# Kernel optimization log

Measured on AMD Instinct MI355X. Metric: run time of the kernel, lower is better.

## Reference

```python
import jax, jax.numpy as jnp
import numpy as np

# Static configuration (uniform ragged layout: every sequence has the same lengths)
B = 8          # number of sequences
QLEN = 256     # new query tokens per sequence
D = 1024       # embedding_dim
H = 16         # num_attention_heads
HD = D // H    # head dim = 64
FFN = 4096     # ffn_embedding_dim
PAGE = 16      # KV-cache page size
KV_TOTAL = 4096            # total KV length per sequence (prefix + new)
P = KV_TOTAL // PAGE       # pages per sequence = 256
NEW_PAGES = QLEN // PAGE   # pages occupied by the new tokens = 16
NUM_PAGES = B * P          # 2048
PREFIX = KV_TOTAL - QLEN   # cached prefix length per sequence
SCALE = HD ** -0.5
LN_EPS = 1e-5


def layer_norm(x, g, b):
    mu = jnp.mean(x, axis=-1, keepdims=True)
    var = jnp.mean(jnp.square(x - mu), axis=-1, keepdims=True)
    return (x - mu) * jax.lax.rsqrt(var + LN_EPS) * g + b


def setup_inputs() -> dict:
    key = jax.random.key(0)
    ks = jax.random.split(key, 12)
    s = 0.02
    inp = {
        "x": jax.random.normal(ks[0], (B * QLEN, D), jnp.float32),
        "pagetable": jax.random.normal(ks[1], (NUM_PAGES, 2, PAGE, H, HD), jnp.float32) * 0.5,
        "Wq": jax.random.normal(ks[2], (D, D), jnp.float32) * s,
        "bq": jnp.zeros((D,), jnp.float32),
        "Wk": jax.random.normal(ks[3], (D, D), jnp.float32) * s,
        "bk": jnp.zeros((D,), jnp.float32),
        "Wv": jax.random.normal(ks[4], (D, D), jnp.float32) * s,
        "bv": jnp.zeros((D,), jnp.float32),
        "Wo": jax.random.normal(ks[5], (D, D), jnp.float32) * s,
        "bo": jnp.zeros((D,), jnp.float32),
        "ln1_g": jnp.ones((D,), jnp.float32),
        "ln1_b": jnp.zeros((D,), jnp.float32),
        "W1": jax.random.normal(ks[6], (D, FFN), jnp.float32) * s,
        "b1": jnp.zeros((FFN,), jnp.float32),
        "W2": jax.random.normal(ks[7], (FFN, D), jnp.float32) * s,
        "b2": jnp.zeros((D,), jnp.float32),
        "lnf_g": jnp.ones((D,), jnp.float32),
        "lnf_b": jnp.zeros((D,), jnp.float32),
        "qo_indptr": jnp.arange(B + 1, dtype=jnp.int32) * QLEN,
        "paged_kv_indptr": jnp.arange(B + 1, dtype=jnp.int32) * P,
        "paged_kv_indices": jnp.arange(NUM_PAGES, dtype=jnp.int32),
        "paged_kv_last_page_len": jnp.full((B,), PAGE, jnp.int32),
        "layer_idx": 0,
    }
    return inp


def reference(x, pagetable, Wq, bq, Wk, bk, Wv, bv, Wo, bo,
              ln1_g, ln1_b, W1, b1, W2, b2, lnf_g, lnf_b,
              qo_indptr, paged_kv_indptr, paged_kv_indices,
              paged_kv_last_page_len, layer_idx):
    residual = x

    # ---- paged self-attention (post-LN path: layer_norm_first=False) ----
    q = ((x @ Wq + bq) * SCALE).reshape(B, QLEN, H, HD)
    k_new = (x @ Wk + bk).reshape(B, QLEN, H, HD)
    v_new = (x @ Wv + bv).reshape(B, QLEN, H, HD)

    # append new K/V into the last NEW_PAGES pages of each sequence
    page_ids = paged_kv_indices.reshape(B, P)                 # [B, P]
    new_ids = page_ids[:, P - NEW_PAGES:].reshape(-1)         # [B*NEW_PAGES]
    kv_new = jnp.stack([k_new, v_new], axis=2)                # [B, QLEN, 2, H, HD]
    kv_new = kv_new.reshape(B, NEW_PAGES, PAGE, 2, H, HD).transpose(0, 1, 3, 2, 4, 5)
    pt = pagetable.at[new_ids].set(kv_new.reshape(-1, 2, PAGE, H, HD))

    # gather the full paged KV per sequence
    kv = pt[page_ids]                                         # [B, P, 2, PAGE, H, HD]
    K = kv[:, :, 0].reshape(B, KV_TOTAL, H, HD)
    V = kv[:, :, 1].reshape(B, KV_TOTAL, H, HD)

    # streaming-causal mask: query i attends to kv positions <= PREFIX + i
    scores = jnp.einsum("bqhd,bkhd->bhqk", q, K)              # [B, H, QLEN, KV_TOTAL]
    kv_pos = jnp.arange(KV_TOTAL)[None, :]
    q_pos = PREFIX + jnp.arange(QLEN)[:, None]
    scores = jnp.where(kv_pos <= q_pos, scores, jnp.float32(-1e30))
    attn = jax.nn.softmax(scores, axis=-1)
    ctx = jnp.einsum("bhqk,bkhd->bqhd", attn, V).reshape(B * QLEN, D)
    x = ctx @ Wo + bo

    x = residual + x
    x = layer_norm(x, ln1_g, ln1_b)

    # ---- FFN ----
    residual = x
    x = jax.nn.relu(x @ W1 + b1)
    x = x @ W2 + b2
    layer_result = x
    x = residual + x
    x = layer_norm(x, lnf_g, lnf_b)

    return x, layer_result, pt
```

## Files before the change

kernel.cpp:

```cpp
#include <hip/hip_runtime.h>
#include <hip/hip_bf16.h>

typedef unsigned short u16;
typedef __attribute__((ext_vector_type(4))) float f32x4;
typedef __attribute__((ext_vector_type(8))) short short8;

#define MODE_QKV 0
#define MODE_WO  1
#define MODE_F1  2
#define MODE_F2  3

__device__ inline u16 f2bf(float f) {
    __hip_bfloat16 h = __float2bfloat16(f);
    return *(u16*)&h;
}

typedef __attribute__((address_space(3))) unsigned int lds_u32_t;
typedef const __attribute__((address_space(1))) unsigned int glb_u32_t;
__device__ inline void gload16(const u16* g, u16* l) {
    __builtin_amdgcn_global_load_lds((glb_u32_t*)(const void*)g,
                                     (lds_u32_t*)(void*)l, 16, 0, 0);
}

__global__ __launch_bounds__(256) void prep_wx(
    const float* __restrict__ Wq, const float* __restrict__ Wk,
    const float* __restrict__ Wv, const float* __restrict__ x,
    u16* __restrict__ WqkvT, u16* __restrict__ xb) {
    int bid = blockIdx.x;
    int tid = threadIdx.x;
    int tx = tid & 31, ty = tid >> 5;
    if (bid >= 3072) {
        int i = (bid - 3072) * 256 + tid;
        const float4* p = (const float4*)(x + (size_t)i * 8);
        float4 a = p[0], b = p[1];
        u16 t[8] = {f2bf(a.x), f2bf(a.y), f2bf(a.z), f2bf(a.w),
                    f2bf(b.x), f2bf(b.y), f2bf(b.z), f2bf(b.w)};
        *(uint4*)(xb + (size_t)i * 8) = *(const uint4*)t;
        return;
    }
    int m = bid >> 10, r = bid & 1023;
    const float* src = (m == 0) ? Wq : (m == 1) ? Wk : Wv;
    u16* dst = WqkvT + (size_t)m * 1024 * 1024;
    __shared__ float t[32][33];
    int n0 = (r & 31) * 32, k0 = (r >> 5) * 32;
#pragma unroll
    for (int j = 0; j < 32; j += 8)
        t[ty + j][tx] = src[(size_t)(k0 + ty + j) * 1024 + n0 + tx];
    __syncthreads();
#pragma unroll
    for (int j = 0; j < 32; j += 8)
        dst[(size_t)(n0 + ty + j) * 1024 + k0 + tx] = f2bf(t[tx][ty + j]);
}

__global__ __launch_bounds__(256) void ln_wo(const float* __restrict__ p0,
                                             const float* __restrict__ p1,
                                             const float* __restrict__ bo,
                                             const float* __restrict__ resid,
                                             const float* __restrict__ g,
                                             const float* __restrict__ be,
                                             float* __restrict__ outf,
                                             u16* __restrict__ outb) {
    int row = blockIdx.x;
    int tid = threadIdx.x;
    int c = tid * 4;
    size_t o = (size_t)row * 1024 + c;
    f32x4 v = *(const f32x4*)(p0 + o) + *(const f32x4*)(p1 + o)
            + *(const f32x4*)(bo + c) + *(const f32x4*)(resid + o);
    float s = v[0] + v[1] + v[2] + v[3];
#pragma unroll
    for (int m = 1; m < 64; m <<= 1) s += __shfl_xor(s, m, 64);
    __shared__ float red1[4], red2[4];
    int w = tid >> 6;
    if ((tid & 63) == 0) red1[w] = s;
    __syncthreads();
    float mu = (red1[0] + red1[1] + red1[2] + red1[3]) * (1.0f / 1024.0f);
    f32x4 d = v - mu;
    float q = d[0] * d[0] + d[1] * d[1] + d[2] * d[2] + d[3] * d[3];
#pragma unroll
    for (int m = 1; m < 64; m <<= 1) q += __shfl_xor(q, m, 64);
    if ((tid & 63) == 0) red2[w] = q;
    __syncthreads();
    float var = (red2[0] + red2[1] + red2[2] + red2[3]) * (1.0f / 1024.0f);
    float rs = rsqrtf(var + 1e-5f);
    f32x4 gg = *(const f32x4*)(g + c), bb = *(const f32x4*)(be + c);
    f32x4 ov = d * rs * gg + bb;
    *(f32x4*)(outf + o) = ov;
    u16 t[4] = {f2bf(ov[0]), f2bf(ov[1]), f2bf(ov[2]), f2bf(ov[3])};
    *(uint2*)&outb[o] = *(const uint2*)t;
}

__global__ __launch_bounds__(256) void ln_f2(const float* __restrict__ q0,
                                             const float* __restrict__ b2,
                                             const float* __restrict__ xln1f,
                                             const float* __restrict__ g,
                                             const float* __restrict__ be,
                                             float* __restrict__ out_lr,
                                             float* __restrict__ out_x) {
    int row = blockIdx.x;
    int tid = threadIdx.x;
    int c = tid * 4;
    size_t o = (size_t)row * 1024 + c;
    const size_t st = (size_t)2048 * 1024;
    f32x4 v = *(const f32x4*)(q0 + o) + *(const f32x4*)(q0 + st + o)
            + *(const f32x4*)(q0 + 2 * st + o) + *(const f32x4*)(q0 + 3 * st + o)
            + *(const f32x4*)(b2 + c);
    *(f32x4*)(out_lr + o) = v;
    v = v + *(const f32x4*)(xln1f + o);
    float s = v[0] + v[1] + v[2] + v[3];
#pragma unroll
    for (int m = 1; m < 64; m <<= 1) s += __shfl_xor(s, m, 64);
    __shared__ float red1[4], red2[4];
    int w = tid >> 6;
    if ((tid & 63) == 0) red1[w] = s;
    __syncthreads();
    float mu = (red1[0] + red1[1] + red1[2] + red1[3]) * (1.0f / 1024.0f);
    f32x4 d = v - mu;
    float q = d[0] * d[0] + d[1] * d[1] + d[2] * d[2] + d[3] * d[3];
#pragma unroll
    for (int m = 1; m < 64; m <<= 1) q += __shfl_xor(q, m, 64);
    if ((tid & 63) == 0) red2[w] = q;
    __syncthreads();
    float var = (red2[0] + red2[1] + red2[2] + red2[3]) * (1.0f / 1024.0f);
    float rs = rsqrtf(var + 1e-5f);
    f32x4 gg = *(const f32x4*)(g + c), bb = *(const f32x4*)(be + c);
    *(f32x4*)(out_x + o) = d * rs * gg + bb;
}

template <int MODE>
__device__ __forceinline__ void gemm_body(
    u16* As, u16* Bs, int m0, int n0,
    const u16* __restrict__ A, const u16* __restrict__ Bt, int lda, int Kspan, int N,
    const float* __restrict__ bias0, const float* __restrict__ bias1,
    const float* __restrict__ bias2,
    float* __restrict__ o0, u16* __restrict__ ob,
    u16* __restrict__ kbf, u16* __restrict__ vbf, const int* __restrict__ kvidx) {
    int tid = threadIdx.x;
    int l = tid & 63, w = tid >> 6;
    int wr = w >> 1, wc = w & 1;
    int lr = l & 15, lg = l >> 4;
    int lrow8 = l >> 3;
    int scol = ((l & 7) ^ lrow8) << 3;
    f32x4 acc[4][4] = {};
    for (int kb = 0; kb < Kspan; kb += 64) {
#pragma unroll
        for (int p = 0; p < 4; ++p) {
            int chunk = p * 4 + w;
            int r = chunk * 8 + lrow8;
            gload16(&A[(size_t)(m0 + r) * lda + kb + scol], &As[chunk * 512]);
            gload16(&Bt[(size_t)(n0 + r) * lda + kb + scol], &Bs[chunk * 512]);
        }
        __syncthreads();
#pragma unroll
        for (int kk = 0; kk < 2; ++kk) {
            short8 a[4], b[4];
            int c0 = kk * 32 + lg * 8;
#pragma unroll
            for (int mi = 0; mi < 4; mi++) {
                int row = wr * 64 + mi * 16 + lr;
                a[mi] = *(const short8*)&As[row * 64 + (c0 ^ ((row & 7) << 3))];
            }
#pragma unroll
            for (int ni = 0; ni < 4; ni++) {
                int row = wc * 64 + ni * 16 + lr;
                b[ni] = *(const short8*)&Bs[row * 64 + (c0 ^ ((row & 7) << 3))];
            }
#pragma unroll
            for (int mi = 0; mi < 4; mi++)
#pragma unroll
                for (int ni = 0; ni < 4; ni++)
                    acc[mi][ni] = __builtin_amdgcn_mfma_f32_16x16x32_bf16(
                        a[mi], b[ni], acc[mi][ni], 0, 0, 0);
        }
        __syncthreads();
    }
#pragma unroll
    for (int mi = 0; mi < 4; mi++) {
#pragma unroll
        for (int ni = 0; ni < 4; ni++) {
#pragma unroll
            for (int r = 0; r < 4; r++) {
                int row = m0 + wr * 64 + mi * 16 + lg * 4 + r;
                int col = n0 + wc * 64 + ni * 16 + lr;
                float v = acc[mi][ni][r];
                if constexpr (MODE == MODE_QKV) {
                    int sel = col >> 10, c = col & 1023;
                    int b = row >> 8, ii = row & 255;
                    int h = (c >> 6), hd = c & 63;
                    if (sel == 0) {
                        ob[(size_t)row * 1024 + c] = f2bf((v + bias0[c]) * 0.125f);
                    } else if (sel == 1) {
                        float val = v + bias1[c];
                        int page = kvidx[b * 256 + 240 + (ii >> 4)];
                        o0[(size_t)page * 32768 + (size_t)(ii & 15) * 1024 + c] = val;
                        kbf[((size_t)(b * 16 + h) * 4096 + 3840 + ii) * 64 + hd] = f2bf(val);
                    } else {
                        float val = v + bias2[c];
                        int page = kvidx[b * 256 + 240 + (ii >> 4)];
                        o0[(size_t)page * 32768 + 16384 + (size_t)(ii & 15) * 1024 + c] = val;
                        vbf[((size_t)(b * 16 + h) * 64 + hd) * 4096 + 3840 + ii] = f2bf(val);
                    }
                } else if constexpr (MODE == MODE_F1) {
                    float t = v + bias0[col];
                    ob[(size_t)row * N + col] = f2bf(fmaxf(t, 0.0f));
                } else {
                    o0[(size_t)row * N + col] = v;
                }
            }
        }
    }
}

template <int MODE>
__global__ __launch_bounds__(256) void gemm_nt(
    const u16* __restrict__ A, const u16* __restrict__ Bt,
    int lda, int Kspan, int N, int gx, int nper,
    const float* __restrict__ bias0,
    float* __restrict__ o0, u16* __restrict__ ob, size_t osplit) {
    __shared__ __align__(16) u16 smem[128 * 64 * 2];
    int bid = blockIdx.x;
    int split = bid / nper, t = bid % nper;
    gemm_body<MODE>(smem, smem + 128 * 64, (t / gx) * 128, (t % gx) * 128,
                    A + (size_t)split * Kspan, Bt + (size_t)split * Kspan,
                    lda, Kspan, N, bias0, nullptr, nullptr,
                    o0 ? o0 + (size_t)split * osplit : nullptr, ob,
                    nullptr, nullptr, nullptr);
}

__global__ __launch_bounds__(256) void mega_prep(
    const u16* __restrict__ xb, const u16* __restrict__ WqkvT,
    const float* __restrict__ bq, const float* __restrict__ bk,
    const float* __restrict__ bv,
    float* __restrict__ out_pt, u16* __restrict__ qbuf,
    u16* __restrict__ Kbf, u16* __restrict__ Vtbf,
    const float* __restrict__ pgt, const int* __restrict__ kvidx,
    const float* __restrict__ Wo, const float* __restrict__ W1,
    const float* __restrict__ W2,
    u16* __restrict__ WoT, u16* __restrict__ W1T, u16* __restrict__ W2T) {
    __shared__ __align__(16) u16 smem[128 * 64 * 2];
    int bid = blockIdx.x;
    int tid = threadIdx.x;
    if (bid < 480) {
        int tile = bid % 60, b = bid / 60;
        int T0 = tile * 64;
        int h = tid >> 4, hd0 = (tid & 15) * 4;
        int pg[4];
#pragma unroll
        for (int pi = 0; pi < 4; ++pi) pg[pi] = kvidx[b * 256 + (T0 >> 4) + pi];
#pragma unroll 4
        for (int it2 = 0; it2 < 64; ++it2) {
            int pi = it2 >> 4, it = it2 & 15;
            const float* src = pgt + (size_t)pg[pi] * 32768;
            float* dst = out_pt + (size_t)pg[pi] * 32768;
            size_t o = (size_t)it * 1024 + tid * 4;
            float4 f = *(const float4*)(src + o);
            *(float4*)(dst + o) = f;
            u16 k4[4] = {f2bf(f.x), f2bf(f.y), f2bf(f.z), f2bf(f.w)};
            size_t kdst = ((size_t)(b * 16 + h) * 4096 + T0 + pi * 16 + it) * 64 + hd0;
            *(uint2*)&Kbf[kdst] = *(const uint2*)k4;
        }
        return;
    }
    if (bid < 960) {
        int vb2 = bid - 480;
        int tile = vb2 % 60, b = vb2 / 60;
        int T0 = tile * 64;
        int pg[4];
#pragma unroll
        for (int pi = 0; pi < 4; ++pi) pg[pi] = kvidx[b * 256 + (T0 >> 4) + pi];
        u16* vt = smem;
        for (int hb2 = 0; hb2 < 8; ++hb2) {
#pragma unroll 4
            for (int it = 0; it < 8; ++it) {
                int ti = it * 8 + (tid >> 5);
                int pi = ti >> 4, tokloc = ti & 15;
                int c4 = (tid & 31) * 4;
                size_t o = (size_t)pg[pi] * 32768 + 16384 + (size_t)tokloc * 1024
                           + hb2 * 128 + c4;
                float4 v = *(const float4*)(pgt + o);
                *(float4*)(out_pt + o) = v;
                u16 v4[4] = {f2bf(v.x), f2bf(v.y), f2bf(v.z), f2bf(v.w)};
                *(uint2*)&vt[ti * 134 + c4] = *(const uint2*)v4;
            }
            __syncthreads();
            int g = tid >> 4, j = tid & 15;
#pragma unroll
            for (int rp = 0; rp < 8; ++rp) {
                int ri = rp * 16 + g;
                int h = hb2 * 2 + (ri >> 6), hd = ri & 63;
                u16 o4[4];
#pragma unroll
                for (int s = 0; s < 4; ++s) o4[s] = vt[(j * 4 + s) * 134 + ri];
                *(uint2*)&Vtbf[((size_t)(b * 16 + h) * 64 + hd) * 4096 + T0 + j * 4] =
                    *(const uint2*)o4;
            }
            __syncthreads();
        }
        return;
    }
    if (bid < 1344) {
        int t = bid - 960;
        gemm_body<MODE_QKV>(smem, smem + 8192, (t / 24) * 128, (t % 24) * 128,
                            xb, WqkvT, 1024, 1024, 3072, bq, bk, bv,
                            out_pt, qbuf, Kbf, Vtbf, kvidx);
        return;
    }
    int wb = bid - 1344;
    const float* src; u16* dst; int K, N, bx, by;
    if (wb < 1024) {
        bx = wb & 31; by = wb >> 5; K = 1024; N = 1024; src = Wo; dst = WoT;
    } else if (wb < 5120) {
        int r = wb - 1024; bx = r & 127; by = r >> 7; K = 1024; N = 4096; src = W1; dst = W1T;
    } else {
        int r = wb - 5120; bx = r & 31; by = r >> 5; K = 4096; N = 1024; src = W2; dst = W2T;
    }
    float* t = (float*)smem;
    int tx = tid & 31, ty = tid >> 5;
    int n0 = bx * 32, k0 = by * 32;
#pragma unroll
    for (int j = 0; j < 32; j += 8)
        t[(ty + j) * 33 + tx] = src[(size_t)(k0 + ty + j) * N + n0 + tx];
    __syncthreads();
#pragma unroll
    for (int j = 0; j < 32; j += 8)
        dst[(size_t)(n0 + ty + j) * K + k0 + tx] = f2bf(t[tx * 33 + ty + j]);
}

__global__ __launch_bounds__(512) void attn_kernel(const u16* __restrict__ qb,
                                                   const u16* __restrict__ Kbf,
                                                   const u16* __restrict__ Vtbf,
                                                   float* __restrict__ pOct,
                                                   float* __restrict__ pL) {
    __shared__ u16 Ks[64 * 64];
    __shared__ u16 Vt[64 * 64];
    __shared__ u16 Ps[8][16 * 64];
    int bid = blockIdx.x;
    int tid = threadIdx.x;
    int l = tid & 63, w = tid >> 6;
    int lr = l & 15, lg = l >> 4;
    int x = bid & 7, qt = x >> 2, split = x & 3;
    int h = (bid >> 3) & 15, b = bid >> 7;

    int qrow = qt * 128 + w * 16 + lr;
    const u16* qptr = qb + (size_t)(b * 256 + qrow) * 1024 + h * 64 + lg * 8;
    short8 qf0 = *(const short8*)qptr;
    short8 qf1 = *(const short8*)(qptr + 32);

    const u16* kslab = Kbf + (size_t)(b * 16 + h) * 4096 * 64;
    const u16* vslab = Vtbf + (size_t)(b * 16 + h) * 64 * 4096;

    f32x4 octx[4] = {};
    f32x4 lacc = {};
    short8 ones;
#pragma unroll
    for (int jj = 0; jj < 8; jj++) ones[jj] = (short)0x3F80;

    int qbase = 3840 + qt * 128;
    int ntiles = (qbase + 128) >> 6;
    int tstart = split * 16;
    int tend = min(tstart + 16, ntiles);
    int kt0 = tstart * 64, kt1 = tend * 64;

    int srow = tid >> 3, scol8 = (tid & 7) * 8;
    int sdst = srow * 64 + (scol8 ^ ((srow & 7) << 3));
    const u16* kp = kslab + srow * 64 + scol8;
    const u16* vp = vslab + (size_t)srow * 4096 + scol8;

    uint4 kreg = *(const uint4*)(kp + (size_t)kt0 * 64);
    uint4 vreg = *(const uint4*)(vp + kt0);
    for (int kt = kt0; kt < kt1; kt += 64) {
        *(uint4*)&Ks[sdst] = kreg;
        *(uint4*)&Vt[sdst] = vreg;
        __syncthreads();
        bool hn = (kt + 64) < kt1;
        if (hn) {
            kreg = *(const uint4*)(kp + (size_t)(kt + 64) * 64);
            vreg = *(const uint4*)(vp + kt + 64);
        }
        float P[4][4];
        bool need_mask = (kt + 63 > qbase);
#pragma unroll
        for (int ni = 0; ni < 4; ni++) {
            f32x4 s = {};
            int krow = ni * 16 + lr;
            int swz = (krow & 7) << 3;
            short8 k0 = *(const short8*)&Ks[krow * 64 + ((lg * 8) ^ swz)];
            short8 k1 = *(const short8*)&Ks[krow * 64 + ((32 + lg * 8) ^ swz)];
            s = __builtin_amdgcn_mfma_f32_16x16x32_bf16(qf0, k0, s, 0, 0, 0);
            s = __builtin_amdgcn_mfma_f32_16x16x32_bf16(qf1, k1, s, 0, 0, 0);
            if (need_mask) {
                int col = kt + ni * 16 + lr;
#pragma unroll
                for (int r = 0; r < 4; r++) {
                    int q = qt * 128 + w * 16 + lg * 4 + r;
                    P[ni][r] = (col <= 3840 + q) ? __expf(s[r]) : 0.0f;
                }
            } else {
#pragma unroll
                for (int r = 0; r < 4; r++) P[ni][r] = __expf(s[r]);
            }
        }
#pragma unroll
        for (int ni = 0; ni < 4; ni++)
#pragma unroll
            for (int r = 0; r < 4; r++) {
                int prow = lg * 4 + r;
                Ps[w][prow * 64 + ((ni * 16 + lr) ^ ((prow & 7) << 3))] = f2bf(P[ni][r]);
            }
#pragma unroll
        for (int kk = 0; kk < 2; kk++) {
            int c0 = kk * 32 + lg * 8;
            short8 pf = *(const short8*)&Ps[w][lr * 64 + (c0 ^ ((lr & 7) << 3))];
            lacc = __builtin_amdgcn_mfma_f32_16x16x32_bf16(pf, ones, lacc, 0, 0, 0);
#pragma unroll
            for (int dt = 0; dt < 4; dt++) {
                int vrow = dt * 16 + lr;
                short8 vf = *(const short8*)&Vt[vrow * 64 + (c0 ^ ((vrow & 7) << 3))];
                octx[dt] = __builtin_amdgcn_mfma_f32_16x16x32_bf16(pf, vf, octx[dt], 0, 0, 0);
            }
        }
        __syncthreads();
    }
    size_t obase = (((size_t)(split * 8 + b) * 16 + h) * 256 + qt * 128) * 64;
#pragma unroll
    for (int dt = 0; dt < 4; dt++)
#pragma unroll
        for (int r = 0; r < 4; r++)
            pOct[obase + (size_t)(w * 16 + lg * 4 + r) * 64 + dt * 16 + lr] = octx[dt][r];
    if (lr == 0) {
        size_t lbase = ((size_t)(split * 8 + b) * 16 + h) * 256 + qt * 128;
#pragma unroll
        for (int r = 0; r < 4; r++) pL[lbase + w * 16 + lg * 4 + r] = lacc[r];
    }
}

__global__ __launch_bounds__(256) void attn_combine(const float* __restrict__ pOct,
                                                    const float* __restrict__ pL,
                                                    u16* __restrict__ ctxb) {
    int row = blockIdx.x;
    int b = row >> 8, q = row & 255;
    int tid = threadIdx.x;
    int h = tid >> 4, dq = (tid & 15) * 4;
    size_t stride = (size_t)128 * 256 * 64;
    size_t base = ((size_t)(b * 16 + h) * 256 + q) * 64 + dq;
    size_t lstride = 128 * 256;
    size_t lbase = (size_t)(b * 16 + h) * 256 + q;
    f32x4 s = {};
    float ls = 0.0f;
#pragma unroll
    for (int sp = 0; sp < 4; sp++) {
        f32x4 v = *(const f32x4*)(pOct + sp * stride + base);
        s += v;
        ls += pL[sp * lstride + lbase];
    }
    float inv = 1.0f / ls;
    u16 o[4] = {f2bf(s[0] * inv), f2bf(s[1] * inv), f2bf(s[2] * inv), f2bf(s[3] * inv)};
    *(uint2*)&ctxb[(size_t)row * 1024 + h * 64 + dq] = *(const uint2*)o;
}

extern "C" void kernel_launch(void* const* d_in, const int* in_sizes, int n_in,
                              void* d_out, int out_size, void* d_ws, size_t ws_size,
                              hipStream_t stream) {
    (void)in_sizes; (void)n_in; (void)out_size; (void)ws_size;
    const float* x   = (const float*)d_in[0];
    const float* pgt = (const float*)d_in[1];
    const float* Wq  = (const float*)d_in[2];
    const float* bq  = (const float*)d_in[3];
    const float* Wk  = (const float*)d_in[4];
    const float* bk  = (const float*)d_in[5];
    const float* Wv  = (const float*)d_in[6];
    const float* bv  = (const float*)d_in[7];
    const float* Wo  = (const float*)d_in[8];
    const float* bo  = (const float*)d_in[9];
    const float* ln1g = (const float*)d_in[10];
    const float* ln1b = (const float*)d_in[11];
    const float* W1  = (const float*)d_in[12];
    const float* b1  = (const float*)d_in[13];
    const float* W2  = (const float*)d_in[14];
    const float* b2  = (const float*)d_in[15];
    const float* lnfg = (const float*)d_in[16];
    const float* lnfb = (const float*)d_in[17];
    const int* kvidx = (const int*)d_in[20];

    float* out = (float*)d_out;
    float* out_x  = out;
    float* out_lr = out + 2048 * 1024;
    float* out_pt = out + 2 * 2048 * 1024;

    char* ws = (char*)d_ws;
    size_t off = 0;
    auto alloc = [&](size_t bytes) { void* p = ws + off; off += (bytes + 255) & ~(size_t)255; return p; };
    u16* WqkvT = (u16*)alloc((size_t)3072 * 1024 * 2);
    u16* WoT   = (u16*)alloc((size_t)1024 * 1024 * 2);
    u16* W1T   = (u16*)alloc((size_t)4096 * 1024 * 2);
    u16* W2T   = (u16*)alloc((size_t)1024 * 4096 * 2);
    u16* xb    = (u16*)alloc((size_t)2048 * 1024 * 2);
    u16* qbuf  = (u16*)alloc((size_t)2048 * 1024 * 2);
    u16* ctxb  = (u16*)alloc((size_t)2048 * 1024 * 2);
    char* regB = (char*)alloc((size_t)168 * 1024 * 1024);
    u16* Kbf  = (u16*)regB;
    u16* Vtbf = (u16*)(regB + (size_t)64 * 1024 * 1024);
    float* pOct = (float*)(regB + (size_t)128 * 1024 * 1024);
    float* pL   = (float*)(regB + (size_t)162 * 1024 * 1024);
    float* p0    = (float*)regB;
    float* xln1f = (float*)(regB + (size_t)16 * 1024 * 1024);
    u16*   xln1b = (u16*)(regB + (size_t)24 * 1024 * 1024);
    u16*   hb    = (u16*)(regB + (size_t)32 * 1024 * 1024);
    float* q0    = (float*)(regB + (size_t)128 * 1024 * 1024);

    prep_wx<<<4096, 256, 0, stream>>>(Wq, Wk, Wv, x, WqkvT, xb);
    mega_prep<<<10560, 256, 0, stream>>>(xb, WqkvT, bq, bk, bv,
                                         out_pt, qbuf, Kbf, Vtbf, pgt, kvidx,
                                         Wo, W1, W2, WoT, W1T, W2T);
    attn_kernel<<<1024, 512, 0, stream>>>(qbuf, Kbf, Vtbf, pOct, pL);
    attn_combine<<<2048, 256, 0, stream>>>(pOct, pL, ctxb);
    gemm_nt<MODE_WO><<<256, 256, 0, stream>>>(ctxb, WoT, 1024, 512, 1024, 8, 128,
        nullptr, p0, nullptr, (size_t)2048 * 1024);
    ln_wo<<<2048, 256, 0, stream>>>(p0, p0 + (size_t)2048 * 1024, bo, x,
                                    ln1g, ln1b, xln1f, xln1b);
    gemm_nt<MODE_F1><<<512, 256, 0, stream>>>(xln1b, W1T, 1024, 1024, 4096, 32, 512,
        b1, nullptr, hb, 0);
    gemm_nt<MODE_F2><<<512, 256, 0, stream>>>(hb, W2T, 4096, 1024, 1024, 8, 128,
        nullptr, q0, nullptr, (size_t)2048 * 1024);
    ln_f2<<<2048, 256, 0, stream>>>(q0, b2, xln1f, lnfg, lnfb, out_lr, out_x);
}
```

Baseline: 338.5 us.

## Move weight transposes into attention kernel and add MFMA priority hints

```diff
diff --git a/kernel.cpp b/kernel.cpp
--- a/kernel.cpp
+++ b/kernel.cpp
@@ -232,10 +232,7 @@
     const float* __restrict__ bv,
     float* __restrict__ out_pt, u16* __restrict__ qbuf,
     u16* __restrict__ Kbf, u16* __restrict__ Vtbf,
-    const float* __restrict__ pgt, const int* __restrict__ kvidx,
-    const float* __restrict__ Wo, const float* __restrict__ W1,
-    const float* __restrict__ W2,
-    u16* __restrict__ WoT, u16* __restrict__ W1T, u16* __restrict__ W2T) {
+    const float* __restrict__ pgt, const int* __restrict__ kvidx) {
     __shared__ __align__(16) u16 smem[128 * 64 * 2];
     int bid = blockIdx.x;
     int tid = threadIdx.x;
@@ -297,44 +294,51 @@
         }
         return;
     }
-    if (bid < 1344) {
-        int t = bid - 960;
-        gemm_body<MODE_QKV>(smem, smem + 8192, (t / 24) * 128, (t % 24) * 128,
-                            xb, WqkvT, 1024, 1024, 3072, bq, bk, bv,
-                            out_pt, qbuf, Kbf, Vtbf, kvidx);
-        return;
-    }
-    int wb = bid - 1344;
-    const float* src; u16* dst; int K, N, bx, by;
-    if (wb < 1024) {
-        bx = wb & 31; by = wb >> 5; K = 1024; N = 1024; src = Wo; dst = WoT;
-    } else if (wb < 5120) {
-        int r = wb - 1024; bx = r & 127; by = r >> 7; K = 1024; N = 4096; src = W1; dst = W1T;
-    } else {
-        int r = wb - 5120; bx = r & 31; by = r >> 5; K = 4096; N = 1024; src = W2; dst = W2T;
-    }
-    float* t = (float*)smem;
-    int tx = tid & 31, ty = tid >> 5;
-    int n0 = bx * 32, k0 = by * 32;
-#pragma unroll
-    for (int j = 0; j < 32; j += 8)
-        t[(ty + j) * 33 + tx] = src[(size_t)(k0 + ty + j) * N + n0 + tx];
-    __syncthreads();
-#pragma unroll
-    for (int j = 0; j < 32; j += 8)
-        dst[(size_t)(n0 + ty + j) * K + k0 + tx] = f2bf(t[tx * 33 + ty + j]);
+    int t = bid - 960;
+    gemm_body<MODE_QKV>(smem, smem + 8192, (t / 24) * 128, (t % 24) * 128,
+                        xb, WqkvT, 1024, 1024, 3072, bq, bk, bv,
+                        out_pt, qbuf, Kbf, Vtbf, kvidx);
 }
 
 __global__ __launch_bounds__(512) void attn_kernel(const u16* __restrict__ qb,
                                                    const u16* __restrict__ Kbf,
                                                    const u16* __restrict__ Vtbf,
                                                    float* __restrict__ pOct,
-                                                   float* __restrict__ pL) {
+                                                   float* __restrict__ pL,
+                                                   const float* __restrict__ Wo,
+                                                   const float* __restrict__ W1,
+                                                   const float* __restrict__ W2,
+                                                   u16* __restrict__ WoT,
+                                                   u16* __restrict__ W1T,
+                                                   u16* __restrict__ W2T) {
     __shared__ u16 Ks[64 * 64];
     __shared__ u16 Vt[64 * 64];
     __shared__ u16 Ps[8][16 * 64];
     int bid = blockIdx.x;
     int tid = threadIdx.x;
+    if (bid >= 1024) {
+        int sub = tid >> 8, t2 = tid & 255;
+        int wb = (bid - 1024) * 2 + sub;
+        const float* src; u16* dst; int K, N, bx, by;
+        if (wb < 1024) {
+            bx = wb & 31; by = wb >> 5; K = 1024; N = 1024; src = Wo; dst = WoT;
+        } else if (wb < 5120) {
+            int r = wb - 1024; bx = r & 127; by = r >> 7; K = 1024; N = 4096; src = W1; dst = W1T;
+        } else {
+            int r = wb - 5120; bx = r & 31; by = r >> 5; K = 4096; N = 1024; src = W2; dst = W2T;
+        }
+        float* t = sub ? (float*)Vt : (float*)Ks;
+        int tx = t2 & 31, ty = t2 >> 5;
+        int n0 = bx * 32, k0 = by * 32;
+#pragma unroll
+        for (int jj = 0; jj < 32; jj += 8)
+            t[(ty + jj) * 33 + tx] = src[(size_t)(k0 + ty + jj) * N + n0 + tx];
+        __syncthreads();
+#pragma unroll
+        for (int jj = 0; jj < 32; jj += 8)
+            dst[(size_t)(n0 + ty + jj) * K + k0 + tx] = f2bf(t[tx * 33 + ty + jj]);
+        return;
+    }
     int l = tid & 63, w = tid >> 6;
     int lr = l & 15, lg = l >> 4;
     int x = bid & 7, qt = x >> 2, split = x & 3;
@@ -378,6 +382,7 @@
         }
         float P[4][4];
         bool need_mask = (kt + 63 > qbase);
+        __builtin_amdgcn_s_setprio(1);
 #pragma unroll
         for (int ni = 0; ni < 4; ni++) {
             f32x4 s = {};
@@ -399,6 +404,7 @@
                 for (int r = 0; r < 4; r++) P[ni][r] = __expf(s[r]);
             }
         }
+        __builtin_amdgcn_s_setprio(0);
 #pragma unroll
         for (int ni = 0; ni < 4; ni++)
 #pragma unroll
@@ -406,6 +412,7 @@
                 int prow = lg * 4 + r;
                 Ps[w][prow * 64 + ((ni * 16 + lr) ^ ((prow & 7) << 3))] = f2bf(P[ni][r]);
             }
+        __builtin_amdgcn_s_setprio(1);
 #pragma unroll
         for (int kk = 0; kk < 2; kk++) {
             int c0 = kk * 32 + lg * 8;
@@ -418,6 +425,7 @@
                 octx[dt] = __builtin_amdgcn_mfma_f32_16x16x32_bf16(pf, vf, octx[dt], 0, 0, 0);
             }
         }
+        __builtin_amdgcn_s_setprio(0);
         __syncthreads();
     }
     size_t obase = (((size_t)(split * 8 + b) * 16 + h) * 256 + qt * 128) * 64;
@@ -508,10 +516,10 @@
     float* q0    = (float*)(regB + (size_t)128 * 1024 * 1024);
 
     prep_wx<<<4096, 256, 0, stream>>>(Wq, Wk, Wv, x, WqkvT, xb);
-    mega_prep<<<10560, 256, 0, stream>>>(xb, WqkvT, bq, bk, bv,
-                                         out_pt, qbuf, Kbf, Vtbf, pgt, kvidx,
-                                         Wo, W1, W2, WoT, W1T, W2T);
-    attn_kernel<<<1024, 512, 0, stream>>>(qbuf, Kbf, Vtbf, pOct, pL);
+    mega_prep<<<1344, 256, 0, stream>>>(xb, WqkvT, bq, bk, bv,
+                                        out_pt, qbuf, Kbf, Vtbf, pgt, kvidx);
+    attn_kernel<<<5632, 512, 0, stream>>>(qbuf, Kbf, Vtbf, pOct, pL,
+                                          Wo, W1, W2, WoT, W1T, W2T);
     attn_combine<<<2048, 256, 0, stream>>>(pOct, pL, ctxb);
     gemm_nt<MODE_WO><<<256, 256, 0, stream>>>(ctxb, WoT, 1024, 512, 1024, 8, 128,
         nullptr, p0, nullptr, (size_t)2048 * 1024);
```

Result: faster. 330.7 us (-2.3%).
